# Kernel tuning notes

Hardware: AMD Instinct MI355X
Metric: run time of the kernel (lower is better)

The kernel has to match this reference:

```python
import jax, jax.numpy as jnp
import numpy as np
from jax.scipy.linalg import expm

ORDER = 256
SEQ_LEN = 4096
THETA = 4096.0
MEMORY_D = 4
INPUT_SIZE = 256
HIDDEN = 512
BATCH = 8


def _lmu_AB(order):
    # Continuous-time LMU (Legendre) state-space matrices
    q = np.arange(order, dtype=np.float64)
    r = 2.0 * q + 1.0
    i, j = np.meshgrid(q, q, indexing="ij")
    A = np.where(i < j, -1.0, (-1.0) ** (i - j + 1)) * r[:, None]
    B = ((-1.0) ** q * r)[:, None]
    return A, B


def _discretize_zoh(A, B, dt=1.0):
    # ZOH via augmented matrix exponential: expm([[A,B],[0,0]]*dt)
    n = A.shape[0]
    M = np.zeros((n + 1, n + 1))
    M[:n, :n] = A * dt
    M[:n, n:] = B * dt
    Md = expm(jnp.asarray(M, dtype=jnp.float64) if jax.config.jax_enable_x64 else jnp.asarray(M, dtype=jnp.float32))
    return Md[:n, :n].astype(jnp.float32), Md[:n, n:].astype(jnp.float32)


def _impulse_H(order, seq_len, theta):
    A, B = _lmu_AB(order)
    Ad, Bd = _discretize_zoh(A / theta, B / theta, 1.0)

    def step(A_i, _):
        # H_t = A^t B ; emit A_i @ Bd then advance A_i <- Ad @ A_i
        return Ad @ A_i, (A_i @ Bd)[:, 0]

    _, Hs = jax.lax.scan(step, jnp.eye(order, dtype=jnp.float32), None, length=seq_len)
    return Hs.T  # [order, seq_len]


def setup_inputs() -> dict:
    key = jax.random.key(0)
    k1, k2, k3, k4, k5 = jax.random.split(key, 5)
    x = jax.random.normal(k1, (BATCH, SEQ_LEN, INPUT_SIZE), dtype=jnp.float32)
    Wu_w = jax.random.normal(k2, (MEMORY_D, INPUT_SIZE), dtype=jnp.float32) * (1.0 / np.sqrt(INPUT_SIZE))
    Wu_b = jax.random.normal(k3, (MEMORY_D,), dtype=jnp.float32) * 0.01
    msz = MEMORY_D * ORDER + INPUT_SIZE
    Wh_w = jax.random.normal(k4, (HIDDEN, msz), dtype=jnp.float32) * (1.0 / np.sqrt(msz))
    Wh_b = jax.random.normal(k5, (HIDDEN,), dtype=jnp.float32) * 0.01
    H = _impulse_H(ORDER, SEQ_LEN, THETA)  # exact LMU impulse response buffer
    return {"x": x, "Wu_w": Wu_w, "Wu_b": Wu_b, "Wh_w": Wh_w, "Wh_b": Wh_b, "H": H}


def reference(x, Wu_w, Wu_b, Wh_w, Wh_b, H):
    B, L, _ = x.shape
    u = jax.nn.relu(x @ Wu_w.T + Wu_b)                     # [B, L, memory_d]
    fft_u = jnp.fft.rfft(u.transpose(0, 2, 1), n=2 * L, axis=-1)   # [B, md, L+1]
    fft_H = jnp.fft.rfft(H, n=2 * L, axis=-1)              # [order, L+1]
    temp = fft_u[:, :, None, :] * fft_H[None, None, :, :]  # [B, md, order, L+1]
    m = jnp.fft.irfft(temp, n=2 * L, axis=-1)[..., :L]     # [B, md, order, L]
    m = m.reshape(B, -1, L).transpose(0, 2, 1)             # [B, L, md*order]
    input_h = jnp.concatenate([m, x], axis=-1)             # [B, L, md*order + input]
    h = jax.nn.relu(input_h @ Wh_w.T + Wh_b)               # [B, L, hidden]
    return h, h[:, -1, :]
```

## Files before the change

### kernel.cpp

```cpp
#include <hip/hip_runtime.h>

#define NB 8
#define LSEQ 4096
#define INS 256
#define MD 4
#define ORD 256
#define HID 512
#define MSZ 1280
#define FS 4128
#define NSPEC 8256
#define GMT 1056768
#define GNT 16384

#define PD(n) ((n) + ((n) >> 3))
#define LDSN 4608

typedef __attribute__((ext_vector_type(8))) short short8;
typedef __attribute__((ext_vector_type(4))) float floatx4;

struct ush4 { unsigned short x, y, z, w; };

__device__ float2 g_tw4096[4096];
__device__ float2 g_tw8192[4098];

__device__ __forceinline__ unsigned short f2bf(float f) {
    unsigned u = __float_as_uint(f);
    u += 0x7FFF + ((u >> 16) & 1);
    return (unsigned short)(u >> 16);
}
__device__ __forceinline__ ush4 pack4(float4 v) {
    ush4 p; p.x = f2bf(v.x); p.y = f2bf(v.y); p.z = f2bf(v.z); p.w = f2bf(v.w); return p;
}
__device__ __forceinline__ float bf2f(unsigned short s) {
    return __uint_as_float(((unsigned)s) << 16);
}

__device__ __forceinline__ float2 cmul(float2 a, float2 b) {
    return make_float2(fmaf(a.x, b.x, -(a.y * b.y)), fmaf(a.x, b.y, a.y * b.x));
}
__device__ __forceinline__ float2 cadd(float2 a, float2 b) { return make_float2(a.x + b.x, a.y + b.y); }
__device__ __forceinline__ float2 csub(float2 a, float2 b) { return make_float2(a.x - b.x, a.y - b.y); }

template <int DIR>
__device__ __forceinline__ float2 jmul(float2 z) {
    return (DIR < 0) ? make_float2(z.y, -z.x) : make_float2(-z.y, z.x);
}

template <int DIR, int N_, int S_>
__device__ __forceinline__ void fft_stage_ip(float2* __restrict__ X, int tid) {
    constexpr int M_ = N_ / 8;
    constexpr int STEP = 4096 / N_;
    const int q = tid & (S_ - 1);
    const int p = tid / S_;
    const int rb = q + S_ * p;
    const float2 a0 = X[PD(rb + S_ * 0 * M_)];
    const float2 a1 = X[PD(rb + S_ * 1 * M_)];
    const float2 a2 = X[PD(rb + S_ * 2 * M_)];
    const float2 a3 = X[PD(rb + S_ * 3 * M_)];
    const float2 a4 = X[PD(rb + S_ * 4 * M_)];
    const float2 a5 = X[PD(rb + S_ * 5 * M_)];
    const float2 a6 = X[PD(rb + S_ * 6 * M_)];
    const float2 a7 = X[PD(rb + S_ * 7 * M_)];

    const int pw = p * STEP;
    float2 w[7];
#pragma unroll
    for (int j = 1; j <= 7; ++j) {
        float2 t = g_tw4096[pw * j];
        if (DIR > 0) t.y = -t.y;
        w[j - 1] = t;
    }

    const float2 e0 = cadd(a0, a4), e1 = csub(a0, a4);
    const float2 e2 = cadd(a2, a6), e3 = jmul<DIR>(csub(a2, a6));
    const float2 E0 = cadd(e0, e2), E2 = csub(e0, e2);
    const float2 E1 = cadd(e1, e3), E3 = csub(e1, e3);
    const float2 f0 = cadd(a1, a5), f1 = csub(a1, a5);
    const float2 f2 = cadd(a3, a7), f3 = jmul<DIR>(csub(a3, a7));
    const float2 O0 = cadd(f0, f2), O2 = csub(f0, f2);
    const float2 O1 = cadd(f1, f3), O3 = csub(f1, f3);

    constexpr float C707 = 0.70710678118654752440f;
    const float2 W1 = make_float2(C707, DIR * C707);
    const float2 W3 = make_float2(-C707, DIR * C707);
    const float2 T1 = cmul(O1, W1);
    const float2 T2 = jmul<DIR>(O2);
    const float2 T3 = cmul(O3, W3);

    const float2 b0 = cadd(E0, O0), b4 = csub(E0, O0);
    const float2 b1 = cadd(E1, T1), b5 = csub(E1, T1);
    const float2 b2 = cadd(E2, T2), b6 = csub(E2, T2);
    const float2 b3 = cadd(E3, T3), b7 = csub(E3, T3);

    __syncthreads();

    const int wb = q + S_ * 8 * p;
    X[PD(wb + 0 * S_)] = b0;
    X[PD(wb + 1 * S_)] = cmul(b1, w[0]);
    X[PD(wb + 2 * S_)] = cmul(b2, w[1]);
    X[PD(wb + 3 * S_)] = cmul(b3, w[2]);
    X[PD(wb + 4 * S_)] = cmul(b4, w[3]);
    X[PD(wb + 5 * S_)] = cmul(b5, w[4]);
    X[PD(wb + 6 * S_)] = cmul(b6, w[5]);
    X[PD(wb + 7 * S_)] = cmul(b7, w[6]);
    __syncthreads();
}

template <int DIR>
__device__ __forceinline__ void fft4096_ip(float2* A, int tid) {
    __syncthreads();
    fft_stage_ip<DIR, 4096, 1>(A, tid);
    fft_stage_ip<DIR, 512, 8>(A, tid);
    fft_stage_ip<DIR, 64, 64>(A, tid);
    fft_stage_ip<DIR, 8, 512>(A, tid);
}

extern "C" __global__ __launch_bounds__(256) void u_relu_k(
    const float* __restrict__ x, const float* __restrict__ Wuw,
    const float* __restrict__ Wub, float* __restrict__ u_t,
    unsigned short* __restrict__ x_bf,
    const float* __restrict__ Whw, unsigned short* __restrict__ Whw_bf) {
    const int blk = blockIdx.x;
    if (blk >= 8832) {
        if (blk < 8848) {
            const int i = (blk - 8832) * 256 + threadIdx.x;
            float sn, cs;
            sincosf(-1.53398078788564403e-3f * (float)i, &sn, &cs);
            g_tw4096[i] = make_float2(cs, sn);
        } else {
            const int i = (blk - 8848) * 256 + threadIdx.x;
            if (i <= 4097) {
                float sn, cs;
                sincosf(-7.66990393942820614e-4f * (float)i, &sn, &cs);
                g_tw8192[i] = make_float2(cs, sn);
            }
        }
        return;
    }
    if (blk >= 8192) {
        const int idx = (blk - 8192) * 256 + threadIdx.x;
        const float4 v = ((const float4*)Whw)[idx];
        *(ush4*)(&Whw_bf[(size_t)idx * 4]) = pack4(v);
        return;
    }
    const int gid = blk * 256 + threadIdx.x;
    const int row = gid >> 6;
    const int lane = threadIdx.x & 63;
    const float4 xv = ((const float4*)x)[(size_t)row * 64 + lane];
    unsigned d0 = (unsigned)f2bf(xv.x) | ((unsigned)f2bf(xv.y) << 16);
    unsigned d1 = (unsigned)f2bf(xv.z) | ((unsigned)f2bf(xv.w) << 16);
    const unsigned e0 = (unsigned)__shfl_xor((int)d0, 1);
    const unsigned e1 = (unsigned)__shfl_xor((int)d1, 1);
    if (!(lane & 1)) {
        uint4 v; v.x = d0; v.y = d1; v.z = e0; v.w = e1;
        *(uint4*)(&x_bf[(size_t)row * 256 + lane * 4]) = v;
    }
    const float4 w0 = ((const float4*)Wuw)[0 * 64 + lane];
    const float4 w1 = ((const float4*)Wuw)[1 * 64 + lane];
    const float4 w2 = ((const float4*)Wuw)[2 * 64 + lane];
    const float4 w3 = ((const float4*)Wuw)[3 * 64 + lane];
    float a0 = xv.x * w0.x + xv.y * w0.y + xv.z * w0.z + xv.w * w0.w;
    float a1 = xv.x * w1.x + xv.y * w1.y + xv.z * w1.z + xv.w * w1.w;
    float a2 = xv.x * w2.x + xv.y * w2.y + xv.z * w2.z + xv.w * w2.w;
    float a3 = xv.x * w3.x + xv.y * w3.y + xv.z * w3.z + xv.w * w3.w;
#pragma unroll
    for (int off = 1; off < 64; off <<= 1) {
        a0 += __shfl_xor(a0, off);
        a1 += __shfl_xor(a1, off);
        a2 += __shfl_xor(a2, off);
        a3 += __shfl_xor(a3, off);
    }
    if (lane < 4) {
        float v = (lane == 0) ? a0 : (lane == 1) ? a1 : (lane == 2) ? a2 : a3;
        v = fmaxf(v + Wub[lane], 0.0f);
        const int b = row >> 12, t = row & 4095;
        u_t[((size_t)(b * 4 + lane)) * LSEQ + t] = v;
    }
}

extern "C" __global__ __launch_bounds__(512) void rfft_all_k(
    const float* __restrict__ ut, const float* __restrict__ H,
    float2* __restrict__ fftU, unsigned short* __restrict__ fftHB) {
    __shared__ float2 A[LDSN];
    const int blk = blockIdx.x;
    const int tid = threadIdx.x;
    const bool is_u = (blk < 32);
    const float* src = is_u ? (ut + (size_t)blk * LSEQ) : (H + (size_t)(blk - 32) * LSEQ);
    const float2* rp = (const float2*)src;
#pragma unroll
    for (int j = 0; j < 8; ++j) {
        const int n = tid + j * 512;
        A[PD(n)] = (n < 2048) ? rp[n] : make_float2(0.f, 0.f);
    }
    fft4096_ip<-1>(A, tid);
    if (is_u) {
        float2* op = fftU + (size_t)blk * FS;
#pragma unroll
        for (int j = 0; j < 9; ++j) {
            const int k = tid + j * 512;
            if (k <= 4096) {
                const float2 Zk = A[PD(k & 4095)];
                const float2 Zm = A[PD((4096 - k) & 4095)];
                const float2 E = make_float2(0.5f * (Zk.x + Zm.x), 0.5f * (Zk.y - Zm.y));
                const float2 D = make_float2(0.5f * (Zk.x - Zm.x), 0.5f * (Zk.y + Zm.y));
                const float2 O = make_float2(D.y, -D.x);
                const float2 t = g_tw8192[k];
                op[k] = cadd(E, cmul(t, O));
            }
        }
    } else {
        const int o = blk - 32;
        unsigned* op = (unsigned*)(fftHB + (size_t)o * NSPEC);
#pragma unroll
        for (int j = 0; j < 9; ++j) {
            const int k = tid + j * 512;
            if (k <= 4096) {
                const float2 Zk = A[PD(k & 4095)];
                const float2 Zm = A[PD((4096 - k) & 4095)];
                const float2 E = make_float2(0.5f * (Zk.x + Zm.x), 0.5f * (Zk.y - Zm.y));
                const float2 D = make_float2(0.5f * (Zk.x - Zm.x), 0.5f * (Zk.y + Zm.y));
                const float2 O = make_float2(D.y, -D.x);
                const float2 t = g_tw8192[k];
                const float2 c = cadd(E, cmul(t, O));
                if (2 * k < NSPEC)
                    op[k] = (unsigned)f2bf(c.x) | ((unsigned)f2bf(c.y) << 16);
            }
        }
    }
}

extern "C" __global__ __launch_bounds__(256) void ht2_k(
    const unsigned short* __restrict__ fftHB, unsigned short* __restrict__ fftHT) {
    __shared__ unsigned short T[64 * 68];
    const int tid = threadIdx.x;
    const int s0 = blockIdx.x * 64;
    const int o0 = blockIdx.y * 64;
    const int r = tid >> 4, c4 = (tid & 15) * 4;
#pragma unroll
    for (int i = 0; i < 4; ++i) {
        const int o = r + 16 * i;
        const ush4 v = *(const ush4*)(fftHB + (size_t)(o0 + o) * NSPEC + s0 + c4);
        *(ush4*)(&T[o * 68 + c4]) = v;
    }
    __syncthreads();
#pragma unroll
    for (int i = 0; i < 4; ++i) {
        const int sl = r + 16 * i;
        const int s = s0 + sl;
        ush4 p;
        if (s < 8194) {
            p.x = T[(c4 + 0) * 68 + sl];
            p.y = T[(c4 + 1) * 68 + sl];
            p.z = T[(c4 + 2) * 68 + sl];
            p.w = T[(c4 + 3) * 68 + sl];
        } else { p.x = p.y = p.z = p.w = 0; }
        *(ush4*)(&fftHT[(size_t)s * 256 + o0 + c4]) = p;
    }
}

extern "C" __global__ __launch_bounds__(256) void g_gemm_k(
    const unsigned short* __restrict__ Whw_bf, const unsigned short* __restrict__ fftHT,
    unsigned short* __restrict__ fftG) {
    __shared__ __align__(16) char smem[36864];
    short* As = (short*)smem;
    short* Bs = (short*)(smem + 18432);
    short* Tt = (short*)smem;

    const int tid = threadIdx.x, lane = tid & 63, wave = tid >> 6;
    const int wg = blockIdx.x;
    const int loc = wg >> 3;
    const int mt = (wg & 7) * 2 + (loc & 1);
    const int nt = loc >> 1;
    const int m0 = mt * 128;
    const int n0 = nt * 128;
    floatx4 acc[2][8];
#pragma unroll
    for (int i = 0; i < 2; ++i)
#pragma unroll
        for (int j = 0; j < 8; ++j) acc[i][j] = (floatx4){0.f, 0.f, 0.f, 0.f};

    const int lr = tid >> 3;
    const int lc = (tid & 7) * 8;
    short8 ra[4], rb[4];

#define GL_A(kc, i) (*(const short8*)(Whw_bf + (size_t)((m0 + lr + 32 * (i)) >> 2) * MSZ + ((m0 + lr + 32 * (i)) & 3) * 256 + (kc) * 64 + lc))
#pragma unroll
    for (int i = 0; i < 4; ++i) {
        ra[i] = GL_A(0, i);
        const int n = n0 + lr + 32 * i;
        rb[i] = (n < NSPEC) ? *(const short8*)(fftHT + (size_t)n * 256 + lc)
                            : (short8){0, 0, 0, 0, 0, 0, 0, 0};
    }

    for (int kc = 0; kc < 4; ++kc) {
#pragma unroll
        for (int i = 0; i < 4; ++i) {
            *(short8*)(&As[(lr + 32 * i) * 72 + lc]) = ra[i];
            *(short8*)(&Bs[(lr + 32 * i) * 72 + lc]) = rb[i];
        }
        __syncthreads();
        if (kc < 3) {
#pragma unroll
            for (int i = 0; i < 4; ++i) {
                ra[i] = GL_A(kc + 1, i);
                const int n = n0 + lr + 32 * i;
                rb[i] = (n < NSPEC) ? *(const short8*)(fftHT + (size_t)n * 256 + (kc + 1) * 64 + lc)
                                    : (short8){0, 0, 0, 0, 0, 0, 0, 0};
            }
        }
        const int arow = (wave * 32 + (lane & 15)) * 72;
        const int brow = (lane & 15) * 72;
        const int kq = 8 * (lane >> 4);
#pragma unroll
        for (int kk = 0; kk < 2; ++kk) {
            const int ko = kk * 32 + kq;
            const short8 a0 = *(const short8*)(&As[arow + ko]);
            const short8 a1 = *(const short8*)(&As[arow + 16 * 72 + ko]);
#pragma unroll
            for (int nf = 0; nf < 8; ++nf) {
                const short8 bv = *(const short8*)(&Bs[brow + nf * 16 * 72 + ko]);
                acc[0][nf] = __builtin_amdgcn_mfma_f32_16x16x32_bf16(a0, bv, acc[0][nf], 0, 0, 0);
                acc[1][nf] = __builtin_amdgcn_mfma_f32_16x16x32_bf16(a1, bv, acc[1][nf], 0, 0, 0);
            }
        }
        __syncthreads();
    }
#undef GL_A
    const int wm = wave * 32;
#pragma unroll
    for (int mf = 0; mf < 2; ++mf) {
        const int row = wm + mf * 16 + 4 * (lane >> 4);
#pragma unroll
        for (int nf = 0; nf < 8; ++nf) {
            const int col = nf * 16 + (lane & 15);
#pragma unroll
            for (int r = 0; r < 4; ++r)
                Tt[(row + r) * 136 + col] = (short)f2bf(acc[mf][nf][r]);
        }
    }
    __syncthreads();
    const size_t gb = (size_t)mt * GMT + (size_t)nt * GNT;
    if (n0 < 8192) {
#pragma unroll
        for (int i = 0; i < 8; ++i) {
            const int idx = tid + i * 256;
            const int ml = idx >> 4, c8 = (idx & 15) * 8;
            const short8 v = *(const short8*)(&Tt[ml * 136 + c8]);
            *(short8*)(&fftG[gb + (size_t)idx * 8]) = v;
        }
    } else {
#pragma unroll
        for (int i = 0; i < 4; ++i) {
            const int idx = tid + i * 256;
            const int ml = idx >> 3, c8 = (idx & 7) * 8;
            const short8 v = *(const short8*)(&Tt[ml * 136 + c8]);
            *(short8*)(&fftG[gb + (size_t)idx * 8]) = v;
        }
    }
}

extern "C" __global__ __launch_bounds__(512) void conv_ifft_k(
    const float2* __restrict__ fftU, const unsigned short* __restrict__ fftG,
    unsigned short* __restrict__ y) {
    __shared__ float2 A[LDSN];
    __shared__ float2 S4096;
    const int wg = blockIdx.x;
    const int h = ((wg & 7) << 6) + (wg >> 6);
    const int b = (wg >> 3) & 7;
    const int tid = threadIdx.x;
    const float2* U = fftU + (size_t)b * MD * FS;
    const size_t mbase = (size_t)(h >> 5) * GMT + (size_t)((h & 31) * 4) * 128;
    const size_t tail = (size_t)(h >> 5) * GMT + (size_t)64 * GNT + (size_t)((h & 31) * 4) * 64;
#pragma unroll
    for (int j = 0; j < 9; ++j) {
        const int k = tid + j * 512;
        if (k <= 4096) {
            float2 s = make_float2(0.f, 0.f);
#pragma unroll
            for (int d = 0; d < MD; ++d) {
                const unsigned gv = (k < 4096)
                    ? *(const unsigned*)(fftG + mbase + (size_t)d * 128 + (size_t)(k >> 6) * GNT + (k & 63) * 2)
                    : *(const unsigned*)(fftG + tail + (size_t)d * 64);
                const float2 uu = U[d * FS + k];
                const float gx = __uint_as_float(gv << 16);
                const float gy = __uint_as_float(gv & 0xFFFF0000u);
                s.x = fmaf(uu.x, gx, fmaf(-uu.y, gy, s.x));
                s.y = fmaf(uu.x, gy, fmaf(uu.y, gx, s.y));
            }
            if (k < 4096) A[PD(k)] = s;
            else S4096 = s;
        }
    }
    __syncthreads();
    float2 Sk[8], Sm[8];
#pragma unroll
    for (int j = 0; j < 8; ++j) {
        const int k = tid + j * 512;
        Sk[j] = A[PD(k)];
        Sm[j] = (k == 0) ? S4096 : A[PD(4096 - k)];
    }
    __syncthreads();
#pragma unroll
    for (int j = 0; j < 8; ++j) {
        const int k = tid + j * 512;
        const float2 E = make_float2(0.5f * (Sk[j].x + Sm[j].x), 0.5f * (Sk[j].y - Sm[j].y));
        const float2 D = make_float2(0.5f * (Sk[j].x - Sm[j].x), 0.5f * (Sk[j].y + Sm[j].y));
        const float2 t = g_tw8192[k];
        const float2 tc = make_float2(t.x, -t.y);
        const float2 O = cmul(D, tc);
        A[PD(k)] = make_float2(E.x - O.y, E.y + O.x);
    }
    fft4096_ip<1>(A, tid);
    unsigned short* yp = y + (size_t)(b * HID + h) * LSEQ;
    const float inv = 1.0f / 4096.0f;
    {
        const int q = tid;
        unsigned dw[4];
#pragma unroll
        for (int jj = 0; jj < 4; ++jj) {
            const float2 z = A[PD(4 * q + jj)];
            dw[jj] = (unsigned)f2bf(z.x * inv) | ((unsigned)f2bf(z.y * inv) << 16);
        }
        uint4 v; v.x = dw[0]; v.y = dw[1]; v.z = dw[2]; v.w = dw[3];
        *(uint4*)(yp + 8 * q) = v;
    }
}

extern "C" __global__ __launch_bounds__(256) void out_gemm_k(
    const unsigned short* __restrict__ x_bf, const unsigned short* __restrict__ Whw_bf,
    const float* __restrict__ Whb, const unsigned short* __restrict__ y,
    float* __restrict__ out) {
    __shared__ __align__(16) char smem[36864];
    short* As = (short*)smem;
    short* Bs = (short*)(smem + 18432);
    float* Ys = (float*)smem;
    float* Ct = (float*)smem;

    const int tid = threadIdx.x, lane = tid & 63, wave = tid >> 6;
    const int wg = blockIdx.x;
    const int s = ((wg & 7) << 7) + (wg >> 3);
    const int m0 = (s >> 2) * 128;
    const int h0 = (s & 3) * 128;
    const int b = m0 >> 12;
    const int t0 = m0 & 4095;

    floatx4 acc[2][8];
#pragma unroll
    for (int i = 0; i < 2; ++i)
#pragma unroll
        for (int j = 0; j < 8; ++j) acc[i][j] = (floatx4){0.f, 0.f, 0.f, 0.f};

    const int lr = tid >> 3;
    const int lc = (tid & 7) * 8;
    const unsigned short* Ap = x_bf + (size_t)(m0 + lr) * INS + lc;
    const unsigned short* Bp = Whw_bf + (size_t)(h0 + lr) * MSZ + 1024 + lc;
    short8 ra[4], rb[4];
#pragma unroll
    for (int i = 0; i < 4; ++i) {
        ra[i] = *(const short8*)(Ap + (size_t)(32 * i) * INS);
        rb[i] = *(const short8*)(Bp + (size_t)(32 * i) * MSZ);
    }

    for (int kc = 0; kc < 4; ++kc) {
#pragma unroll
        for (int i = 0; i < 4; ++i) {
            *(short8*)(&As[(lr + 32 * i) * 72 + lc]) = ra[i];
            *(short8*)(&Bs[(lr + 32 * i) * 72 + lc]) = rb[i];
        }
        __syncthreads();
        if (kc < 3) {
#pragma unroll
            for (int i = 0; i < 4; ++i) {
                ra[i] = *(const short8*)(Ap + (size_t)(32 * i) * INS + (kc + 1) * 64);
                rb[i] = *(const short8*)(Bp + (size_t)(32 * i) * MSZ + (kc + 1) * 64);
            }
        }
        const int arow = (wave * 32 + (lane & 15)) * 72;
        const int brow = (lane & 15) * 72;
        const int kq = 8 * (lane >> 4);
#pragma unroll
        for (int kk = 0; kk < 2; ++kk) {
            const int ko = kk * 32 + kq;
            const short8 a0 = *(const short8*)(&As[arow + ko]);
            const short8 a1 = *(const short8*)(&As[arow + 16 * 72 + ko]);
#pragma unroll
            for (int nf = 0; nf < 8; ++nf) {
                const short8 bv = *(const short8*)(&Bs[brow + nf * 16 * 72 + ko]);
                acc[0][nf] = __builtin_amdgcn_mfma_f32_16x16x32_bf16(a0, bv, acc[0][nf], 0, 0, 0);
                acc[1][nf] = __builtin_amdgcn_mfma_f32_16x16x32_bf16(a1, bv, acc[1][nf], 0, 0, 0);
            }
        }
        __syncthreads();
    }

    const int wm = wave * 32;
    const int yr = tid >> 5, yc = (tid & 31) * 4;
#pragma unroll 1
    for (int half = 0; half < 2; ++half) {
        __syncthreads();
#pragma unroll
        for (int i = 0; i < 8; ++i) {
            const int hh = yr + 8 * i;
            const ush4 v = *(const ush4*)(y + (size_t)(b * HID + h0 + half * 64 + hh) * LSEQ + t0 + yc);
            Ys[hh * 132 + yc + 0] = bf2f(v.x);
            Ys[hh * 132 + yc + 1] = bf2f(v.y);
            Ys[hh * 132 + yc + 2] = bf2f(v.z);
            Ys[hh * 132 + yc + 3] = bf2f(v.w);
        }
        __syncthreads();
        float v[4][2][4];
#pragma unroll
        for (int nfl = 0; nfl < 4; ++nfl) {
            const int nf = half * 4 + nfl;
            const int hh = nfl * 16 + (lane & 15);
            const float bias = Whb[h0 + half * 64 + hh];
#pragma unroll
            for (int mf = 0; mf < 2; ++mf)
#pragma unroll
                for (int r = 0; r < 4; ++r) {
                    const int row = wm + mf * 16 + 4 * (lane >> 4) + r;
                    v[nfl][mf][r] = fmaxf(acc[mf][nf][r] + Ys[hh * 132 + row] + bias, 0.f);
                }
        }
        __syncthreads();
#pragma unroll
        for (int nfl = 0; nfl < 4; ++nfl) {
            const int nloc = nfl * 16 + (lane & 15);
#pragma unroll
            for (int mf = 0; mf < 2; ++mf)
#pragma unroll
                for (int r = 0; r < 4; ++r) {
                    const int row = wm + mf * 16 + 4 * (lane >> 4) + r;
                    Ct[row * 68 + nloc] = v[nfl][mf][r];
                }
        }
        __syncthreads();
#pragma unroll
        for (int i = 0; i < 8; ++i) {
            const int idx = tid + i * 256;
            const int row = idx >> 4, f4 = idx & 15;
            const floatx4 t = *(const floatx4*)&Ct[row * 68 + f4 * 4];
            *(floatx4*)(out + (size_t)(m0 + row) * HID + h0 + half * 64 + f4 * 4) = t;
            if (((m0 + row) & 4095) == 4095)
                *(floatx4*)(out + (size_t)NB * LSEQ * HID + (size_t)b * HID + h0 + half * 64 + f4 * 4) = t;
        }
    }
}

extern "C" void kernel_launch(void* const* d_in, const int* in_sizes, int n_in,
                              void* d_out, int out_size, void* d_ws, size_t ws_size,
                              hipStream_t stream) {
    const float* x   = (const float*)d_in[0];
    const float* Wuw = (const float*)d_in[1];
    const float* Wub = (const float*)d_in[2];
    const float* Whw = (const float*)d_in[3];
    const float* Whb = (const float*)d_in[4];
    const float* H   = (const float*)d_in[5];
    char* wsb = (char*)d_ws;
    unsigned short* fftG   = (unsigned short*)(wsb);
    unsigned short* yb     = (unsigned short*)(wsb + 33816576);
    float*          fftU   = (float*)(wsb + 67371008);
    unsigned short* fftHT  = (unsigned short*)(wsb + 68427776);
    float*          ut     = (float*)(wsb + 72654848);
    unsigned short* x_bf   = (unsigned short*)(wsb + 73179136);
    unsigned short* Whw_bf = (unsigned short*)(wsb + 89956352);
    unsigned short* fftHB  = (unsigned short*)(wsb + 91267072);
    float* out = (float*)d_out;

    hipLaunchKernelGGL(u_relu_k, dim3(8865), dim3(256), 0, stream, x, Wuw, Wub, ut, x_bf, Whw, Whw_bf);
    hipLaunchKernelGGL(rfft_all_k, dim3(288), dim3(512), 0, stream, ut, H, (float2*)fftU, fftHB);
    hipLaunchKernelGGL(ht2_k, dim3(129, 4), dim3(256), 0, stream, fftHB, fftHT);
    hipLaunchKernelGGL(g_gemm_k, dim3(1040), dim3(256), 0, stream, Whw_bf, fftHT, fftG);
    hipLaunchKernelGGL(conv_ifft_k, dim3(4096), dim3(512), 0, stream,
                       (const float2*)fftU, fftG, yb);
    hipLaunchKernelGGL(out_gemm_k, dim3(1024), dim3(256), 0, stream, x_bf, Whw_bf, Whb, yb, out);
}
```

Baseline: 281.3 us.

## Fuse FFT first stages with loads, prune zero-pad, and retile output GEMM

```diff
diff --git a/kernel.cpp b/kernel.cpp
--- a/kernel.cpp
+++ b/kernel.cpp
@@ -46,6 +46,28 @@
     return (DIR < 0) ? make_float2(z.y, -z.x) : make_float2(-z.y, z.x);
 }
 
+template <int DIR>
+__device__ __forceinline__ void bfly8(const float2* a, float2* b) {
+    const float2 e0 = cadd(a[0], a[4]), e1 = csub(a[0], a[4]);
+    const float2 e2 = cadd(a[2], a[6]), e3 = jmul<DIR>(csub(a[2], a[6]));
+    const float2 E0 = cadd(e0, e2), E2 = csub(e0, e2);
+    const float2 E1 = cadd(e1, e3), E3 = csub(e1, e3);
+    const float2 f0 = cadd(a[1], a[5]), f1 = csub(a[1], a[5]);
+    const float2 f2 = cadd(a[3], a[7]), f3 = jmul<DIR>(csub(a[3], a[7]));
+    const float2 O0 = cadd(f0, f2), O2 = csub(f0, f2);
+    const float2 O1 = cadd(f1, f3), O3 = csub(f1, f3);
+    constexpr float C707 = 0.70710678118654752440f;
+    const float2 W1 = make_float2(C707, DIR * C707);
+    const float2 W3 = make_float2(-C707, DIR * C707);
+    const float2 T1 = cmul(O1, W1);
+    const float2 T2 = jmul<DIR>(O2);
+    const float2 T3 = cmul(O3, W3);
+    b[0] = cadd(E0, O0); b[4] = csub(E0, O0);
+    b[1] = cadd(E1, T1); b[5] = csub(E1, T1);
+    b[2] = cadd(E2, T2); b[6] = csub(E2, T2);
+    b[3] = cadd(E3, T3); b[7] = csub(E3, T3);
+}
+
 template <int DIR, int N_, int S_>
 __device__ __forceinline__ void fft_stage_ip(float2* __restrict__ X, int tid) {
     constexpr int M_ = N_ / 8;
@@ -53,14 +75,9 @@
     const int q = tid & (S_ - 1);
     const int p = tid / S_;
     const int rb = q + S_ * p;
-    const float2 a0 = X[PD(rb + S_ * 0 * M_)];
-    const float2 a1 = X[PD(rb + S_ * 1 * M_)];
-    const float2 a2 = X[PD(rb + S_ * 2 * M_)];
-    const float2 a3 = X[PD(rb + S_ * 3 * M_)];
-    const float2 a4 = X[PD(rb + S_ * 4 * M_)];
-    const float2 a5 = X[PD(rb + S_ * 5 * M_)];
-    const float2 a6 = X[PD(rb + S_ * 6 * M_)];
-    const float2 a7 = X[PD(rb + S_ * 7 * M_)];
+    float2 a[8], b[8];
+#pragma unroll
+    for (int l = 0; l < 8; ++l) a[l] = X[PD(rb + S_ * l * M_)];
 
     const int pw = p * STEP;
     float2 w[7];
@@ -71,55 +88,24 @@
         w[j - 1] = t;
     }
 
-    const float2 e0 = cadd(a0, a4), e1 = csub(a0, a4);
-    const float2 e2 = cadd(a2, a6), e3 = jmul<DIR>(csub(a2, a6));
-    const float2 E0 = cadd(e0, e2), E2 = csub(e0, e2);
-    const float2 E1 = cadd(e1, e3), E3 = csub(e1, e3);
-    const float2 f0 = cadd(a1, a5), f1 = csub(a1, a5);
-    const float2 f2 = cadd(a3, a7), f3 = jmul<DIR>(csub(a3, a7));
-    const float2 O0 = cadd(f0, f2), O2 = csub(f0, f2);
-    const float2 O1 = cadd(f1, f3), O3 = csub(f1, f3);
-
-    constexpr float C707 = 0.70710678118654752440f;
-    const float2 W1 = make_float2(C707, DIR * C707);
-    const float2 W3 = make_float2(-C707, DIR * C707);
-    const float2 T1 = cmul(O1, W1);
-    const float2 T2 = jmul<DIR>(O2);
-    const float2 T3 = cmul(O3, W3);
-
-    const float2 b0 = cadd(E0, O0), b4 = csub(E0, O0);
-    const float2 b1 = cadd(E1, T1), b5 = csub(E1, T1);
-    const float2 b2 = cadd(E2, T2), b6 = csub(E2, T2);
-    const float2 b3 = cadd(E3, T3), b7 = csub(E3, T3);
+    bfly8<DIR>(a, b);
 
     __syncthreads();
 
     const int wb = q + S_ * 8 * p;
-    X[PD(wb + 0 * S_)] = b0;
-    X[PD(wb + 1 * S_)] = cmul(b1, w[0]);
-    X[PD(wb + 2 * S_)] = cmul(b2, w[1]);
-    X[PD(wb + 3 * S_)] = cmul(b3, w[2]);
-    X[PD(wb + 4 * S_)] = cmul(b4, w[3]);
-    X[PD(wb + 5 * S_)] = cmul(b5, w[4]);
-    X[PD(wb + 6 * S_)] = cmul(b6, w[5]);
-    X[PD(wb + 7 * S_)] = cmul(b7, w[6]);
-    __syncthreads();
-}
-
-template <int DIR>
-__device__ __forceinline__ void fft4096_ip(float2* A, int tid) {
-    __syncthreads();
-    fft_stage_ip<DIR, 4096, 1>(A, tid);
-    fft_stage_ip<DIR, 512, 8>(A, tid);
-    fft_stage_ip<DIR, 64, 64>(A, tid);
-    fft_stage_ip<DIR, 8, 512>(A, tid);
+    X[PD(wb + 0 * S_)] = b[0];
+#pragma unroll
+    for (int j = 1; j < 8; ++j)
+        X[PD(wb + j * S_)] = cmul(b[j], w[j - 1]);
+    __syncthreads();
 }
 
 extern "C" __global__ __launch_bounds__(256) void u_relu_k(
     const float* __restrict__ x, const float* __restrict__ Wuw,
     const float* __restrict__ Wub, float* __restrict__ u_t,
     unsigned short* __restrict__ x_bf,
-    const float* __restrict__ Whw, unsigned short* __restrict__ Whw_bf) {
+    const float* __restrict__ Whw, unsigned short* __restrict__ Whw_bf,
+    unsigned short* __restrict__ Wt) {
     const int blk = blockIdx.x;
     if (blk >= 8832) {
         if (blk < 8848) {
@@ -137,9 +123,19 @@
         }
         return;
     }
+    if (blk >= 8704) {
+        const int didx = (blk - 8704) * 1024 + threadIdx.x * 4;
+        const int c = didx >> 14;
+        const int r = didx & 16383;
+        const int h = r >> 5, kk = r & 31;
+        const float4 v = *(const float4*)(Whw + (size_t)h * MSZ + 1024 + c * 32 + kk);
+        *(ush4*)(&Wt[didx]) = pack4(v);
+        return;
+    }
     if (blk >= 8192) {
         const int idx = (blk - 8192) * 256 + threadIdx.x;
-        const float4 v = ((const float4*)Whw)[idx];
+        const int h = idx >> 8, c = idx & 255;
+        const float4 v = ((const float4*)Whw)[(size_t)h * 320 + c];
         *(ush4*)(&Whw_bf[(size_t)idx * 4]) = pack4(v);
         return;
     }
@@ -187,12 +183,22 @@
     const bool is_u = (blk < 32);
     const float* src = is_u ? (ut + (size_t)blk * LSEQ) : (H + (size_t)(blk - 32) * LSEQ);
     const float2* rp = (const float2*)src;
-#pragma unroll
-    for (int j = 0; j < 8; ++j) {
-        const int n = tid + j * 512;
-        A[PD(n)] = (n < 2048) ? rp[n] : make_float2(0.f, 0.f);
-    }
-    fft4096_ip<-1>(A, tid);
+    {
+        float2 c[8], b[8];
+#pragma unroll
+        for (int j = 0; j < 4; ++j) c[j] = rp[tid + j * 512];
+#pragma unroll
+        for (int j = 4; j < 8; ++j) c[j] = make_float2(0.f, 0.f);
+        bfly8<-1>(c, b);
+        A[PD(8 * tid + 0)] = b[0];
+#pragma unroll
+        for (int j = 1; j < 8; ++j)
+            A[PD(8 * tid + j)] = cmul(b[j], g_tw4096[tid * j]);
+    }
+    __syncthreads();
+    fft_stage_ip<-1, 512, 8>(A, tid);
+    fft_stage_ip<-1, 64, 64>(A, tid);
+    fft_stage_ip<-1, 8, 512>(A, tid);
     if (is_u) {
         float2* op = fftU + (size_t)blk * FS;
 #pragma unroll
@@ -283,7 +289,7 @@
     const int lc = (tid & 7) * 8;
     short8 ra[4], rb[4];
 
-#define GL_A(kc, i) (*(const short8*)(Whw_bf + (size_t)((m0 + lr + 32 * (i)) >> 2) * MSZ + ((m0 + lr + 32 * (i)) & 3) * 256 + (kc) * 64 + lc))
+#define GL_A(kc, i) (*(const short8*)(Whw_bf + (size_t)((m0 + lr + 32 * (i)) >> 2) * 1024 + ((m0 + lr + 32 * (i)) & 3) * 256 + (kc) * 64 + lc))
 #pragma unroll
     for (int i = 0; i < 4; ++i) {
         ra[i] = GL_A(0, i);
@@ -392,34 +398,49 @@
         }
     }
     __syncthreads();
-    float2 Sk[8], Sm[8];
+    float2 c[8], bt[8];
 #pragma unroll
     for (int j = 0; j < 8; ++j) {
         const int k = tid + j * 512;
-        Sk[j] = A[PD(k)];
-        Sm[j] = (k == 0) ? S4096 : A[PD(4096 - k)];
-    }
-    __syncthreads();
-#pragma unroll
-    for (int j = 0; j < 8; ++j) {
-        const int k = tid + j * 512;
-        const float2 E = make_float2(0.5f * (Sk[j].x + Sm[j].x), 0.5f * (Sk[j].y - Sm[j].y));
-        const float2 D = make_float2(0.5f * (Sk[j].x - Sm[j].x), 0.5f * (Sk[j].y + Sm[j].y));
+        const float2 Sk = A[PD(k)];
+        const float2 Sm = (k == 0) ? S4096 : A[PD(4096 - k)];
+        const float2 E = make_float2(0.5f * (Sk.x + Sm.x), 0.5f * (Sk.y - Sm.y));
+        const float2 D = make_float2(0.5f * (Sk.x - Sm.x), 0.5f * (Sk.y + Sm.y));
         const float2 t = g_tw8192[k];
         const float2 tc = make_float2(t.x, -t.y);
         const float2 O = cmul(D, tc);
-        A[PD(k)] = make_float2(E.x - O.y, E.y + O.x);
-    }
-    fft4096_ip<1>(A, tid);
+        c[j] = make_float2(E.x - O.y, E.y + O.x);
+    }
+    __syncthreads();
+    bfly8<1>(c, bt);
+    A[PD(8 * tid + 0)] = bt[0];
+#pragma unroll
+    for (int j = 1; j < 8; ++j) {
+        float2 t = g_tw4096[tid * j]; t.y = -t.y;
+        A[PD(8 * tid + j)] = cmul(bt[j], t);
+    }
+    __syncthreads();
+    fft_stage_ip<1, 512, 8>(A, tid);
+    fft_stage_ip<1, 64, 64>(A, tid);
+    {
+        float2 z[8], bo[8];
+#pragma unroll
+        for (int k = 0; k < 8; ++k) z[k] = A[PD(tid + 512 * k)];
+        bfly8<1>(z, bo);
+        const float inv = 1.0f / 4096.0f;
+#pragma unroll
+        for (int k = 0; k < 4; ++k)
+            A[PD(tid + 512 * k)] = make_float2(bo[k].x * inv, bo[k].y * inv);
+    }
+    __syncthreads();
     unsigned short* yp = y + (size_t)(b * HID + h) * LSEQ;
-    const float inv = 1.0f / 4096.0f;
     {
         const int q = tid;
         unsigned dw[4];
 #pragma unroll
         for (int jj = 0; jj < 4; ++jj) {
             const float2 z = A[PD(4 * q + jj)];
-            dw[jj] = (unsigned)f2bf(z.x * inv) | ((unsigned)f2bf(z.y * inv) << 16);
+            dw[jj] = (unsigned)f2bf(z.x) | ((unsigned)f2bf(z.y) << 16);
         }
         uint4 v; v.x = dw[0]; v.y = dw[1]; v.z = dw[2]; v.w = dw[3];
         *(uint4*)(yp + 8 * q) = v;
@@ -427,22 +448,23 @@
 }
 
 extern "C" __global__ __launch_bounds__(256) void out_gemm_k(
-    const unsigned short* __restrict__ x_bf, const unsigned short* __restrict__ Whw_bf,
+    const unsigned short* __restrict__ x_bf, const unsigned short* __restrict__ Wt,
     const float* __restrict__ Whb, const unsigned short* __restrict__ y,
     float* __restrict__ out) {
-    __shared__ __align__(16) char smem[36864];
+    __shared__ __align__(16) char smem[66560];
     short* As = (short*)smem;
-    short* Bs = (short*)(smem + 18432);
-    float* Ys = (float*)smem;
+    short* Bs = (short*)(smem + 2560);
+    float* Whbs = (float*)smem;
+    short* Ys = (short*)(smem + 2560);
     float* Ct = (float*)smem;
 
     const int tid = threadIdx.x, lane = tid & 63, wave = tid >> 6;
     const int wg = blockIdx.x;
     const int s = ((wg & 7) << 7) + (wg >> 3);
-    const int m0 = (s >> 2) * 128;
-    const int h0 = (s & 3) * 128;
+    const int m0 = s * 32;
     const int b = m0 >> 12;
     const int t0 = m0 & 4095;
+    const int hq = wave * 128;
 
     floatx4 acc[2][8];
 #pragma unroll
@@ -450,100 +472,80 @@
 #pragma unroll
         for (int j = 0; j < 8; ++j) acc[i][j] = (floatx4){0.f, 0.f, 0.f, 0.f};
 
-    const int lr = tid >> 3;
-    const int lc = (tid & 7) * 8;
-    const unsigned short* Ap = x_bf + (size_t)(m0 + lr) * INS + lc;
-    const unsigned short* Bp = Whw_bf + (size_t)(h0 + lr) * MSZ + 1024 + lc;
-    short8 ra[4], rb[4];
-#pragma unroll
-    for (int i = 0; i < 4; ++i) {
-        ra[i] = *(const short8*)(Ap + (size_t)(32 * i) * INS);
-        rb[i] = *(const short8*)(Bp + (size_t)(32 * i) * MSZ);
-    }
-
-    for (int kc = 0; kc < 4; ++kc) {
-#pragma unroll
-        for (int i = 0; i < 4; ++i) {
-            *(short8*)(&As[(lr + 32 * i) * 72 + lc]) = ra[i];
-            *(short8*)(&Bs[(lr + 32 * i) * 72 + lc]) = rb[i];
-        }
+    short8 ra, rb[8];
+    const int arow = tid >> 2, acb = (tid & 3) * 8;
+    if (tid < 128) ra = *(const short8*)(x_bf + (size_t)(m0 + arow) * INS + acb);
+#pragma unroll
+    for (int j = 0; j < 8; ++j)
+        rb[j] = *(const short8*)(Wt + (size_t)tid * 64 + j * 8);
+
+    for (int c = 0; c < 8; ++c) {
+        if (tid < 128) *(short8*)(&As[arow * 40 + acb]) = ra;
+#pragma unroll
+        for (int j = 0; j < 8; ++j)
+            *(short8*)(&Bs[(2 * tid + (j >> 2)) * 40 + (j & 3) * 8]) = rb[j];
         __syncthreads();
-        if (kc < 3) {
-#pragma unroll
-            for (int i = 0; i < 4; ++i) {
-                ra[i] = *(const short8*)(Ap + (size_t)(32 * i) * INS + (kc + 1) * 64);
-                rb[i] = *(const short8*)(Bp + (size_t)(32 * i) * MSZ + (kc + 1) * 64);
-            }
-        }
-        const int arow = (wave * 32 + (lane & 15)) * 72;
-        const int brow = (lane & 15) * 72;
+        if (c < 7) {
+            if (tid < 128) ra = *(const short8*)(x_bf + (size_t)(m0 + arow) * INS + (c + 1) * 32 + acb);
+#pragma unroll
+            for (int j = 0; j < 8; ++j)
+                rb[j] = *(const short8*)(Wt + (size_t)(c + 1) * 16384 + (size_t)tid * 64 + j * 8);
+        }
         const int kq = 8 * (lane >> 4);
-#pragma unroll
-        for (int kk = 0; kk < 2; ++kk) {
-            const int ko = kk * 32 + kq;
-            const short8 a0 = *(const short8*)(&As[arow + ko]);
-            const short8 a1 = *(const short8*)(&As[arow + 16 * 72 + ko]);
-#pragma unroll
-            for (int nf = 0; nf < 8; ++nf) {
-                const short8 bv = *(const short8*)(&Bs[brow + nf * 16 * 72 + ko]);
-                acc[0][nf] = __builtin_amdgcn_mfma_f32_16x16x32_bf16(a0, bv, acc[0][nf], 0, 0, 0);
-                acc[1][nf] = __builtin_amdgcn_mfma_f32_16x16x32_bf16(a1, bv, acc[1][nf], 0, 0, 0);
-            }
+        const short8 a0 = *(const short8*)(&As[(lane & 15) * 40 + kq]);
+        const short8 a1 = *(const short8*)(&As[((lane & 15) + 16) * 40 + kq]);
+#pragma unroll
+        for (int nf = 0; nf < 8; ++nf) {
+            const short8 bv = *(const short8*)(&Bs[(hq + nf * 16 + (lane & 15)) * 40 + kq]);
+            acc[0][nf] = __builtin_amdgcn_mfma_f32_16x16x32_bf16(a0, bv, acc[0][nf], 0, 0, 0);
+            acc[1][nf] = __builtin_amdgcn_mfma_f32_16x16x32_bf16(a1, bv, acc[1][nf], 0, 0, 0);
         }
         __syncthreads();
     }
 
-    const int wm = wave * 32;
-    const int yr = tid >> 5, yc = (tid & 31) * 4;
-#pragma unroll 1
-    for (int half = 0; half < 2; ++half) {
-        __syncthreads();
-#pragma unroll
-        for (int i = 0; i < 8; ++i) {
-            const int hh = yr + 8 * i;
-            const ush4 v = *(const ush4*)(y + (size_t)(b * HID + h0 + half * 64 + hh) * LSEQ + t0 + yc);
-            Ys[hh * 132 + yc + 0] = bf2f(v.x);
-            Ys[hh * 132 + yc + 1] = bf2f(v.y);
-            Ys[hh * 132 + yc + 2] = bf2f(v.z);
-            Ys[hh * 132 + yc + 3] = bf2f(v.w);
-        }
-        __syncthreads();
-        float v[4][2][4];
-#pragma unroll
-        for (int nfl = 0; nfl < 4; ++nfl) {
-            const int nf = half * 4 + nfl;
-            const int hh = nfl * 16 + (lane & 15);
-            const float bias = Whb[h0 + half * 64 + hh];
-#pragma unroll
-            for (int mf = 0; mf < 2; ++mf)
-#pragma unroll
-                for (int r = 0; r < 4; ++r) {
-                    const int row = wm + mf * 16 + 4 * (lane >> 4) + r;
-                    v[nfl][mf][r] = fmaxf(acc[mf][nf][r] + Ys[hh * 132 + row] + bias, 0.f);
-                }
-        }
-        __syncthreads();
-#pragma unroll
-        for (int nfl = 0; nfl < 4; ++nfl) {
-            const int nloc = nfl * 16 + (lane & 15);
-#pragma unroll
-            for (int mf = 0; mf < 2; ++mf)
-#pragma unroll
-                for (int r = 0; r < 4; ++r) {
-                    const int row = wm + mf * 16 + 4 * (lane >> 4) + r;
-                    Ct[row * 68 + nloc] = v[nfl][mf][r];
-                }
-        }
-        __syncthreads();
-#pragma unroll
-        for (int i = 0; i < 8; ++i) {
-            const int idx = tid + i * 256;
-            const int row = idx >> 4, f4 = idx & 15;
-            const floatx4 t = *(const floatx4*)&Ct[row * 68 + f4 * 4];
-            *(floatx4*)(out + (size_t)(m0 + row) * HID + h0 + half * 64 + f4 * 4) = t;
-            if (((m0 + row) & 4095) == 4095)
-                *(floatx4*)(out + (size_t)NB * LSEQ * HID + (size_t)b * HID + h0 + half * 64 + f4 * 4) = t;
-        }
+    Whbs[tid] = Whb[tid];
+    Whbs[tid + 256] = Whb[tid + 256];
+#pragma unroll
+    for (int i = 0; i < 16; ++i) {
+        const int idx = tid + i * 256;
+        const int hh = idx >> 3, tq = (idx & 7) * 4;
+        const ush4 v = *(const ush4*)(y + (size_t)(b * HID + hh) * LSEQ + t0 + tq);
+        *(ush4*)(&Ys[hh * 36 + tq]) = v;
+    }
+    __syncthreads();
+#pragma unroll
+    for (int nf = 0; nf < 8; ++nf) {
+        const int hh = hq + nf * 16 + (lane & 15);
+        const float bias = Whbs[hh];
+#pragma unroll
+        for (int mf = 0; mf < 2; ++mf)
+#pragma unroll
+            for (int r = 0; r < 4; ++r) {
+                const int row = mf * 16 + 4 * (lane >> 4) + r;
+                acc[mf][nf][r] = fmaxf(acc[mf][nf][r] + bf2f(Ys[hh * 36 + row]) + bias, 0.f);
+            }
+    }
+    __syncthreads();
+#pragma unroll
+    for (int nf = 0; nf < 8; ++nf) {
+        const int col = hq + nf * 16 + (lane & 15);
+#pragma unroll
+        for (int mf = 0; mf < 2; ++mf)
+#pragma unroll
+            for (int r = 0; r < 4; ++r) {
+                const int row = mf * 16 + 4 * (lane >> 4) + r;
+                Ct[row * 520 + col] = acc[mf][nf][r];
+            }
+    }
+    __syncthreads();
+#pragma unroll
+    for (int i = 0; i < 16; ++i) {
+        const int idx = tid + i * 256;
+        const int row = idx >> 7, c4 = (idx & 127) * 4;
+        const floatx4 t = *(const floatx4*)&Ct[row * 520 + c4];
+        *(floatx4*)(out + (size_t)(m0 + row) * HID + c4) = t;
+        if (((m0 + row) & 4095) == 4095)
+            *(floatx4*)(out + (size_t)NB * LSEQ * HID + (size_t)b * HID + c4) = t;
     }
 }
 
@@ -564,14 +566,15 @@
     float*          ut     = (float*)(wsb + 72654848);
     unsigned short* x_bf   = (unsigned short*)(wsb + 73179136);
     unsigned short* Whw_bf = (unsigned short*)(wsb + 89956352);
+    unsigned short* Wt     = (unsigned short*)(wsb + 91004928);
     unsigned short* fftHB  = (unsigned short*)(wsb + 91267072);
     float* out = (float*)d_out;
 
-    hipLaunchKernelGGL(u_relu_k, dim3(8865), dim3(256), 0, stream, x, Wuw, Wub, ut, x_bf, Whw, Whw_bf);
+    hipLaunchKernelGGL(u_relu_k, dim3(8865), dim3(256), 0, stream, x, Wuw, Wub, ut, x_bf, Whw, Whw_bf, Wt);
     hipLaunchKernelGGL(rfft_all_k, dim3(288), dim3(512), 0, stream, ut, H, (float2*)fftU, fftHB);
     hipLaunchKernelGGL(ht2_k, dim3(129, 4), dim3(256), 0, stream, fftHB, fftHT);
     hipLaunchKernelGGL(g_gemm_k, dim3(1040), dim3(256), 0, stream, Whw_bf, fftHT, fftG);
     hipLaunchKernelGGL(conv_ifft_k, dim3(4096), dim3(512), 0, stream,
                        (const float2*)fftU, fftG, yb);
-    hipLaunchKernelGGL(out_gemm_k, dim3(1024), dim3(256), 0, stream, x_bf, Whw_bf, Whb, yb, out);
-}
+    hipLaunchKernelGGL(out_gemm_k, dim3(1024), dim3(256), 0, stream, x_bf, Wt, Whb, yb, out);
+}
```

New measurement: 245.5 us. 12.7% less time.
